# Kernel optimization log

Hardware: AMD Instinct MI355X
Metric: run time of the kernel (lower is better)

The kernel has to match this reference:

```python
import jax, jax.numpy as jnp
import numpy as np

DROPOUT_RATE = 0.6


def dropout(x, key, rate=DROPOUT_RATE):
    keep = jax.random.bernoulli(key, 1.0 - rate, x.shape)
    return jnp.where(keep, x / (1.0 - rate), 0.0).astype(x.dtype)


def gcn_conv(x, W, b, src, dst, n_nodes):
    # h = x @ W  (tiny linear), then symmetric-normalized scatter-add over edges
    h = x @ W                                             # [N, C_out]
    deg = jax.ops.segment_sum(jnp.ones_like(dst, dtype=h.dtype), dst,
                              num_segments=n_nodes)       # in-degree at targets
    dinv = jnp.where(deg > 0, jax.lax.rsqrt(jnp.maximum(deg, 1.0)), 0.0)
    norm = dinv[src] * dinv[dst]                          # [E]
    msg = h[src] * norm[:, None]                          # [E, C_out] gather
    out = jax.ops.segment_sum(msg, dst, num_segments=n_nodes)  # scatter-add
    return out + b


def setup_inputs() -> dict:
    key = jax.random.key(0)
    k_x, k_e, k_w1, k_w2 = jax.random.split(key, 4)
    N, E = 100000, 6400000
    x = jax.random.normal(k_x, (N, 1), dtype=jnp.float32)
    edge_index = jax.random.randint(k_e, (2, E), 0, N, dtype=jnp.int64)
    # GCNConv weights (glorot-ish scale) and zero biases
    W1 = jax.random.normal(k_w1, (1, 16), dtype=jnp.float32) * (1.0 / np.sqrt(1.0))
    b1 = jnp.zeros((16,), dtype=jnp.float32)
    W2 = jax.random.normal(k_w2, (16, 1), dtype=jnp.float32) * (1.0 / np.sqrt(16.0))
    b2 = jnp.zeros((1,), dtype=jnp.float32)
    return {"x": x, "edge_index": edge_index, "W1": W1, "b1": b1, "W2": W2, "b2": b2}


def reference(x, edge_index, W1, b1, W2, b2):
    n_nodes = x.shape[0]
    src, dst = edge_index[0], edge_index[1]
    k1, k2 = jax.random.split(jax.random.key(42), 2)
    h = dropout(x, k1)
    h = gcn_conv(h, W1, b1, src, dst, n_nodes)
    h = jax.nn.relu(h)
    h = dropout(h, k2)
    out = gcn_conv(h, W2, b2, src, dst, n_nodes)
    return out
```

## Files before the change

### kernel.cpp

```cpp
#include <hip/hip_runtime.h>
#include <hip/hip_bf16.h>
#include <stdint.h>


#define KEEP_P 0.4f
#define RANGE 2048
#define SHIFT 11
#define MASK 2047
#define BPC 1024
#define KS 32
#define SEGS (BPC / KS)
#define SPW (SEGS / 4)
#define NBMAX 64
#define TILE 2048
#define TILE4 (TILE / 4)

__host__ __device__ inline unsigned rotl32(unsigned v, int s) {
  return (v << s) | (v >> (32 - s));
}

__host__ __device__ inline void threefry2x32(unsigned key0, unsigned key1,
                                             unsigned x0, unsigned x1,
                                             unsigned& o0, unsigned& o1) {
  unsigned ks0 = key0, ks1 = key1, ks2 = key0 ^ key1 ^ 0x1BD11BDAu;
  unsigned v0 = x0 + ks0, v1 = x1 + ks1;
#define TF_R(r) { v0 += v1; v1 = rotl32(v1, r); v1 ^= v0; }
  TF_R(13) TF_R(15) TF_R(26) TF_R(6)
  v0 += ks1; v1 += ks2 + 1u;
  TF_R(17) TF_R(29) TF_R(16) TF_R(24)
  v0 += ks2; v1 += ks0 + 2u;
  TF_R(13) TF_R(15) TF_R(26) TF_R(6)
  v0 += ks0; v1 += ks1 + 3u;
  TF_R(17) TF_R(29) TF_R(16) TF_R(24)
  v0 += ks1; v1 += ks2 + 4u;
  TF_R(13) TF_R(15) TF_R(26) TF_R(6)
  v0 += ks2; v1 += ks0 + 5u;
#undef TF_R
  o0 = v0; o1 = v1;
}

__device__ inline float u01_from_bits(unsigned bits) {
  return __uint_as_float((bits >> 9) | 0x3f800000u) - 1.0f;
}

__global__ __launch_bounds__(256) void k_part(
    const int* __restrict__ src, const int* __restrict__ dst,
    unsigned* __restrict__ slots, unsigned* __restrict__ cnt,
    int NB, int CAP, int e4, int E) {
  __shared__ unsigned hist[NBMAX], scan_s[NBMAX + 1], off[NBMAX];
  __shared__ unsigned tbase[NBMAX], cur[NBMAX];
  __shared__ unsigned stage[TILE];
  __shared__ unsigned char stage_p[TILE];
  const int tid = threadIdx.x;
  const size_t blkbase = (size_t)blockIdx.x * NB;
  unsigned* myslots = slots + blkbase * CAP;
  for (int p = tid; p < NB; p += 256) cur[p] = (unsigned)(p * CAP);
  const int chunk = (e4 + BPC - 1) / BPC;
  const int j0 = blockIdx.x * chunk;
  const int j1 = min(j0 + chunk, e4);
  const int4* dst4 = reinterpret_cast<const int4*>(dst);
  const int4* src4 = reinterpret_cast<const int4*>(src);

  for (int t0 = j0; t0 < j1; t0 += TILE4) {
    __syncthreads();
    for (int p = tid; p < NB; p += 256) hist[p] = 0u;
    __syncthreads();
    const int ja = t0 + tid, jb = t0 + TILE4 / 2 + tid;
    const bool va = ja < j1 && tid < TILE4 / 2;
    const bool vb = jb < j1;
    int4 da, db;
    if (va) {
      da = dst4[ja];
      atomicAdd(&hist[(unsigned)da.x >> SHIFT], 1u);
      atomicAdd(&hist[(unsigned)da.y >> SHIFT], 1u);
      atomicAdd(&hist[(unsigned)da.z >> SHIFT], 1u);
      atomicAdd(&hist[(unsigned)da.w >> SHIFT], 1u);
    }
    if (vb) {
      db = dst4[jb];
      atomicAdd(&hist[(unsigned)db.x >> SHIFT], 1u);
      atomicAdd(&hist[(unsigned)db.y >> SHIFT], 1u);
      atomicAdd(&hist[(unsigned)db.z >> SHIFT], 1u);
      atomicAdd(&hist[(unsigned)db.w >> SHIFT], 1u);
    }
    __syncthreads();
    if (tid == 0) {
      unsigned acc = 0;
      for (int p = 0; p < NB; ++p) { scan_s[p] = acc; acc += hist[p]; }
      scan_s[NB] = acc;
    }
    __syncthreads();
    for (int p = tid; p < NB; p += 256) {
      off[p] = scan_s[p];
      tbase[p] = cur[p];
      cur[p] += hist[p];
    }
    __syncthreads();
#define STAGE1(d, s) { unsigned ud = (unsigned)(d), us = (unsigned)(s); \
    unsigned p = ud >> SHIFT; unsigned pos = atomicAdd(&off[p], 1u); \
    stage[pos] = (ud & MASK) | (us << SHIFT); stage_p[pos] = (unsigned char)p; }
    if (va) {
      int4 sa = src4[ja];
      STAGE1(da.x, sa.x) STAGE1(da.y, sa.y) STAGE1(da.z, sa.z) STAGE1(da.w, sa.w)
    }
    if (vb) {
      int4 sb = src4[jb];
      STAGE1(db.x, sb.x) STAGE1(db.y, sb.y) STAGE1(db.z, sb.z) STAGE1(db.w, sb.w)
    }
#undef STAGE1
    __syncthreads();
    const int tc = (int)scan_s[NB];
    for (int i = tid; i < tc; i += 256) {
      unsigned p = stage_p[i];
      myslots[tbase[p] + ((unsigned)i - scan_s[p])] = stage[i];
    }
  }
  __syncthreads();
  if (blockIdx.x == 0) {
    for (int t = e4 * 4 + tid; t < E; t += 256) {
      unsigned ud = (unsigned)dst[t], us = (unsigned)src[t];
      unsigned p = ud >> SHIFT;
      unsigned pos = atomicAdd(&cur[p], 1u);
      myslots[pos] = (ud & MASK) | (us << SHIFT);
    }
  }
  __syncthreads();
  for (int p = tid; p < NB; p += 256)
    cnt[blkbase + p] = cur[p] - (unsigned)(p * CAP);
}

__global__ __launch_bounds__(256) void k_deg2(
    const unsigned* __restrict__ slots, const unsigned* __restrict__ cnt,
    unsigned short* __restrict__ part16, int NB, int CAP) {
  __shared__ unsigned bins[RANGE / 2];
  const int tid = threadIdx.x, w = tid >> 6, lane = tid & 63;
  const int p = blockIdx.y, kd = blockIdx.x;
  for (int i = tid; i < RANGE / 2; i += 256) bins[i] = 0u;
  __syncthreads();
  int l[SPW]; const unsigned* e[SPW];
#pragma unroll
  for (int s = 0; s < SPW; ++s) {
    const int b = kd * SEGS + w * SPW + s;
    l[s] = cnt[(size_t)b * NB + p];
    e[s] = slots + ((size_t)b * NB + p) * CAP;
  }
  const int half = lane >> 5, li = lane & 31;
#define DEG_ONE(v) { unsigned r = (v) & MASK; \
    atomicAdd(&bins[r >> 1], 1u << ((r & 1) * 16)); }
#pragma unroll
  for (int r = 0; r < SPW / 2; ++r) {
    const int s = 2 * r + half;
    const unsigned* es = e[s];
    const int ls = l[s];
    const int i1 = 4 * li, i2 = 128 + 4 * li;
    const bool f1 = i1 + 4 <= ls, f2 = i2 + 4 <= ls;
    uint4 u1, u2;
    if (f1) u1 = *reinterpret_cast<const uint4*>(es + i1);
    if (f2) u2 = *reinterpret_cast<const uint4*>(es + i2);
    if (f1) { DEG_ONE(u1.x) DEG_ONE(u1.y) DEG_ONE(u1.z) DEG_ONE(u1.w) }
    if (f2) { DEG_ONE(u2.x) DEG_ONE(u2.y) DEG_ONE(u2.z) DEG_ONE(u2.w) }
  }
  if (lane < SPW) {
    const int s = lane;
    for (int k = l[s] & ~3; k < l[s]; ++k) DEG_ONE(e[s][k])
  }
#undef DEG_ONE
  __syncthreads();
  unsigned* my32 = (unsigned*)(part16 + ((size_t)kd * gridDim.y + p) * RANGE);
  for (int i = tid; i < RANGE / 2; i += 256) my32[i] = bins[i];
}

__global__ __launch_bounds__(256) void k_node1(
    const float* __restrict__ x, const unsigned short* __restrict__ part16,
    float* __restrict__ dinv, float* __restrict__ y,
    int NB, int n, unsigned k1a, unsigned k1b) {
  int i = blockIdx.x * blockDim.x + threadIdx.x;
  if (i >= n) return;
  const int p = i >> SHIFT, r = i & MASK;
  unsigned d = 0;
  for (int b = 0; b < KS; ++b)
    d += part16[((size_t)b * NB + p) * RANGE + r];
  float di = (d > 0) ? (1.0f / sqrtf((float)d)) : 0.0f;
  dinv[i] = di;
  unsigned o0, o1;
  threefry2x32(k1a, k1b, 0u, (unsigned)i, o0, o1);
  float u = u01_from_bits(o0 ^ o1);
  float xd = (u < KEEP_P) ? (x[i] / KEEP_P) : 0.0f;
  y[i] = xd * di;
}

__global__ __launch_bounds__(256) void k_scat(
    const unsigned* __restrict__ slots, const unsigned* __restrict__ cnt,
    const float* __restrict__ val, float* __restrict__ part,
    int NB, int CAP) {
  __shared__ float bins[RANGE];
  const int tid = threadIdx.x, w = tid >> 6, lane = tid & 63;
  const int p = blockIdx.y, ks = blockIdx.x;
  for (int i = tid; i < RANGE; i += 256) bins[i] = 0.0f;
  __syncthreads();
  int l[SPW]; const unsigned* e[SPW];
#pragma unroll
  for (int s = 0; s < SPW; ++s) {
    const int b = ks * SEGS + w * SPW + s;
    l[s] = cnt[(size_t)b * NB + p];
    e[s] = slots + ((size_t)b * NB + p) * CAP;
  }
  const int half = lane >> 5, li = lane & 31;
#pragma unroll
  for (int r = 0; r < SPW / 2; ++r) {
    const int s = 2 * r + half;
    const unsigned* es = e[s];
    const int ls = l[s];
    const int i1 = 4 * li, i2 = 128 + 4 * li;
    const bool f1 = i1 + 4 <= ls, f2 = i2 + 4 <= ls;
    uint4 u1, u2;
    if (f1) u1 = *reinterpret_cast<const uint4*>(es + i1);
    if (f2) u2 = *reinterpret_cast<const uint4*>(es + i2);
    float g0, g1, g2, g3, g4, g5, g6, g7;
    if (f1) {
      g0 = val[u1.x >> SHIFT]; g1 = val[u1.y >> SHIFT];
      g2 = val[u1.z >> SHIFT]; g3 = val[u1.w >> SHIFT];
    }
    if (f2) {
      g4 = val[u2.x >> SHIFT]; g5 = val[u2.y >> SHIFT];
      g6 = val[u2.z >> SHIFT]; g7 = val[u2.w >> SHIFT];
    }
    if (f1) {
      atomicAdd(&bins[u1.x & MASK], g0);
      atomicAdd(&bins[u1.y & MASK], g1);
      atomicAdd(&bins[u1.z & MASK], g2);
      atomicAdd(&bins[u1.w & MASK], g3);
    }
    if (f2) {
      atomicAdd(&bins[u2.x & MASK], g4);
      atomicAdd(&bins[u2.y & MASK], g5);
      atomicAdd(&bins[u2.z & MASK], g6);
      atomicAdd(&bins[u2.w & MASK], g7);
    }
  }
  if (lane < SPW) {
    const int s = lane;
    for (int k = l[s] & ~3; k < l[s]; ++k) {
      unsigned v = e[s][k];
      atomicAdd(&bins[v & MASK], val[v >> SHIFT]);
    }
  }
  __syncthreads();
  float* my = part + ((size_t)ks * NB + p) * RANGE;
  for (int i = tid; i < RANGE; i += 256) my[i] = bins[i];
}

__global__ __launch_bounds__(256) void k_node2(
    const float* __restrict__ part, const float* __restrict__ dinv,
    const float* __restrict__ W1, const float* __restrict__ b1,
    const float* __restrict__ W2, float* __restrict__ z2,
    int NB, int n, unsigned k2a, unsigned k2b) {
  int i = blockIdx.x * blockDim.x + threadIdx.x;
  if (i >= n) return;
  const int p = i >> SHIFT, r = i & MASK;
  float s = 0.0f;
  for (int b = 0; b < KS; ++b)
    s += part[((size_t)b * NB + p) * RANGE + r];
  float t = s * dinv[i];
  float z = 0.0f;
  unsigned base = (unsigned)i * 16u;
#pragma unroll
  for (int c = 0; c < 16; ++c) {
    float h = W1[c] * t + b1[c];
    h = fmaxf(h, 0.0f);
    unsigned o0, o1;
    threefry2x32(k2a, k2b, 0u, base + (unsigned)c, o0, o1);
    float u = u01_from_bits(o0 ^ o1);
    float hd = (u < KEEP_P) ? (h / KEEP_P) : 0.0f;
    z += hd * W2[c];
  }
  z2[i] = z * dinv[i];
}

__global__ __launch_bounds__(256) void k_final(
    const float* __restrict__ part, const float* __restrict__ dinv,
    const float* __restrict__ b2, float* __restrict__ out,
    int NB, int n) {
  int i = blockIdx.x * blockDim.x + threadIdx.x;
  if (i >= n) return;
  const int p = i >> SHIFT, r = i & MASK;
  float s = 0.0f;
  for (int b = 0; b < KS; ++b)
    s += part[((size_t)b * NB + p) * RANGE + r];
  out[i] = b2[0] + dinv[i] * s;
}

extern "C" void kernel_launch(void* const* d_in, const int* in_sizes, int n_in,
                              void* d_out, int out_size, void* d_ws, size_t ws_size,
                              hipStream_t stream) {
  const float* x  = (const float*)d_in[0];
  const int* edge = (const int*)d_in[1];
  const float* W1 = (const float*)d_in[2];
  const float* b1 = (const float*)d_in[3];
  const float* W2 = (const float*)d_in[4];
  const float* b2 = (const float*)d_in[5];
  float* out = (float*)d_out;

  const int N = in_sizes[0];
  const int E = in_sizes[1] / 2;
  const int* src = edge;
  const int* dst = edge + E;

  const int NP = (N + 255) & ~255;
  const int NB = (N + RANGE - 1) / RANGE;

  const size_t cnt_sz  = (size_t)BPC * NB * 4;
  const size_t part_sz = (size_t)KS * NB * RANGE * 4;
  const size_t small_sz = (size_t)3 * NP * 4;
  size_t fixed = cnt_sz + part_sz + small_sz + 512;
  size_t avail = ws_size > fixed ? ws_size - fixed : 0;
  int CAP = (int)(avail / ((size_t)NB * BPC * 4));
  CAP &= ~3;
  if (CAP > 208) CAP = 208;
  if (CAP < 176) CAP = 176;

  char* w = (char*)d_ws;
  unsigned* slots = (unsigned*)w;        w += (size_t)NB * BPC * CAP * 4;
  unsigned* cnt   = (unsigned*)w;        w += cnt_sz;
  w = (char*)(((uintptr_t)w + 255) & ~(uintptr_t)255);
  float* part_f = (float*)w;
  unsigned short* part16 = (unsigned short*)w;
  w += part_sz;
  float* dinv = (float*)w;
  float* y    = dinv + NP;
  float* z2   = y + NP;

  unsigned k1a, k1b, k2a, k2b;
  threefry2x32(0u, 42u, 0u, 0u, k1a, k1b);
  threefry2x32(0u, 42u, 0u, 1u, k2a, k2b);

  const int e4 = E >> 2;
  const int gN = (N + 255) / 256;

  k_part <<<BPC, 256, 0, stream>>>(src, dst, slots, cnt, NB, CAP, e4, E);
  k_deg2 <<<dim3(KS, NB), 256, 0, stream>>>(slots, cnt, part16, NB, CAP);
  k_node1<<<gN, 256, 0, stream>>>(x, part16, dinv, y, NB, N, k1a, k1b);
  k_scat <<<dim3(KS, NB), 256, 0, stream>>>(slots, cnt, y, part_f, NB, CAP);
  k_node2<<<gN, 256, 0, stream>>>(part_f, dinv, W1, b1, W2, z2, NB, N, k2a, k2b);
  k_scat <<<dim3(KS, NB), 256, 0, stream>>>(slots, cnt, z2, part_f, NB, CAP);
  k_final<<<gN, 256, 0, stream>>>(part_f, dinv, b2, out, NB, N);
}
```

Baseline: 223.4 us.

## Add second source-partition pass so scatter gathers node values from shared memory

Adds a second partitioning kernel that regroups the already dst-partitioned edges by source-node window (8192 nodes), writing them into per-(dst-bucket, src-window) slots. The scatter kernels can then stage the source values for one window in LDS and gather from shared memory instead of making random global loads. Degree counting also reads the new layout, and the serial prefix scan in k_part becomes a wave shuffle scan. The cost is an extra full pass over the edge list and more workspace, plus a statistically sized capacity CAP2 that silently drops edges if a bucket overflows.

```diff
diff --git a/kernel.cpp b/kernel.cpp
--- a/kernel.cpp
+++ b/kernel.cpp
@@ -1,6 +1,7 @@
 #include <hip/hip_runtime.h>
 #include <hip/hip_bf16.h>
 #include <stdint.h>
+#include <math.h>
 
 
 #define KEEP_P 0.4f
@@ -8,12 +9,12 @@
 #define SHIFT 11
 #define MASK 2047
 #define BPC 1024
-#define KS 32
-#define SEGS (BPC / KS)
-#define SPW (SEGS / 4)
 #define NBMAX 64
 #define TILE 2048
 #define TILE4 (TILE / 4)
+#define G16 16
+#define ST2 3456
+#define SL 8192
 
 __host__ __device__ inline unsigned rotl32(unsigned v, int s) {
   return (v << s) | (v >> (32 - s));
@@ -46,12 +47,15 @@
 __global__ __launch_bounds__(256) void k_part(
     const int* __restrict__ src, const int* __restrict__ dst,
     unsigned* __restrict__ slots, unsigned* __restrict__ cnt,
-    int NB, int CAP, int e4, int E) {
+    int NB, int CAP, int e4, int E,
+    unsigned* __restrict__ cur2, int nz) {
   __shared__ unsigned hist[NBMAX], scan_s[NBMAX + 1], off[NBMAX];
   __shared__ unsigned tbase[NBMAX], cur[NBMAX];
   __shared__ unsigned stage[TILE];
   __shared__ unsigned char stage_p[TILE];
   const int tid = threadIdx.x;
+  if (blockIdx.x == 0)
+    for (int i = tid; i < nz; i += 256) cur2[i] = 0u;
   const size_t blkbase = (size_t)blockIdx.x * NB;
   unsigned* myslots = slots + blkbase * CAP;
   for (int p = tid; p < NB; p += 256) cur[p] = (unsigned)(p * CAP);
@@ -84,16 +88,22 @@
       atomicAdd(&hist[(unsigned)db.w >> SHIFT], 1u);
     }
     __syncthreads();
-    if (tid == 0) {
-      unsigned acc = 0;
-      for (int p = 0; p < NB; ++p) { scan_s[p] = acc; acc += hist[p]; }
-      scan_s[NB] = acc;
-    }
-    __syncthreads();
-    for (int p = tid; p < NB; p += 256) {
-      off[p] = scan_s[p];
-      tbase[p] = cur[p];
-      cur[p] += hist[p];
+    if (tid < 64) {
+      unsigned h = (tid < NB) ? hist[tid] : 0u;
+      unsigned inc = h;
+#pragma unroll
+      for (int d = 1; d < 64; d <<= 1) {
+        unsigned t = __shfl_up(inc, d, 64);
+        if (tid >= d) inc += t;
+      }
+      if (tid < NB) {
+        unsigned ex = inc - h;
+        scan_s[tid] = ex;
+        off[tid] = ex;
+        tbase[tid] = cur[tid];
+        cur[tid] += h;
+      }
+      if (tid == NB - 1) scan_s[NB] = inc;
     }
     __syncthreads();
 #define STAGE1(d, s) { unsigned ud = (unsigned)(d), us = (unsigned)(s); \
@@ -129,56 +139,112 @@
     cnt[blkbase + p] = cur[p] - (unsigned)(p * CAP);
 }
 
-__global__ __launch_bounds__(256) void k_deg2(
+__global__ __launch_bounds__(256) void k_part2(
     const unsigned* __restrict__ slots, const unsigned* __restrict__ cnt,
-    unsigned short* __restrict__ part16, int NB, int CAP) {
+    unsigned* __restrict__ slots2, unsigned* __restrict__ cur2,
+    int NB, int CAP, int NS, int CAP2) {
+  __shared__ unsigned raw[ST2], stage[ST2];
+  __shared__ unsigned char tagp[ST2];
+  __shared__ unsigned lens_s[G16], offs_s[G16];
+  __shared__ unsigned hist[16], scan_s[16], off[16], gbase[16];
+  __shared__ unsigned tc_s;
+  const int tid = threadIdx.x, wv = tid >> 6, lane = tid & 63;
+  const int p = blockIdx.x, g = blockIdx.y;
+  if (tid < 16) hist[tid] = 0u;
+  if (tid < 64) {
+    unsigned ln = 0;
+    if (lane < G16) {
+      int b = g * G16 + lane;
+      ln = cnt[(size_t)b * NB + p];
+      if (ln > (unsigned)CAP) ln = (unsigned)CAP;
+      lens_s[lane] = ln;
+    }
+    unsigned inc = ln;
+#pragma unroll
+    for (int d = 1; d < 16; d <<= 1) {
+      unsigned t = __shfl_up(inc, d, 64);
+      if (lane >= d) inc += t;
+    }
+    if (lane < G16) offs_s[lane] = inc - ln;
+    if (lane == G16 - 1) tc_s = inc;
+  }
+  __syncthreads();
+  for (int k = 0; k < 4; ++k) {
+    const int j = 4 * wv + k;
+    const unsigned len = lens_s[j], off0 = offs_s[j];
+    const unsigned* e = slots + ((size_t)(g * G16 + j) * NB + p) * CAP;
+    for (unsigned i = lane; i < len; i += 64) raw[off0 + i] = e[i];
+  }
+  __syncthreads();
+  const int TC = (int)tc_s;
+  for (int i = tid; i < TC; i += 256)
+    atomicAdd(&hist[raw[i] >> 24], 1u);
+  __syncthreads();
+  if (tid < 64) {
+    unsigned h = (lane < NS) ? hist[lane] : 0u;
+    unsigned inc = h;
+#pragma unroll
+    for (int d = 1; d < 16; d <<= 1) {
+      unsigned t = __shfl_up(inc, d, 64);
+      if (lane >= d) inc += t;
+    }
+    if (lane < NS) {
+      scan_s[lane] = inc - h;
+      off[lane] = inc - h;
+      gbase[lane] = atomicAdd(&cur2[p * NS + lane], h);
+    }
+  }
+  __syncthreads();
+  for (int i = tid; i < TC; i += 256) {
+    unsigned v = raw[i];
+    unsigned s = v >> 24;
+    unsigned pos = atomicAdd(&off[s], 1u);
+    stage[pos] = (v & MASK) | (((v >> SHIFT) & (SL - 1)) << SHIFT);
+    tagp[pos] = (unsigned char)s;
+  }
+  __syncthreads();
+  for (int i = tid; i < TC; i += 256) {
+    unsigned s = tagp[i];
+    unsigned idx = gbase[s] + ((unsigned)i - scan_s[s]);
+    if (idx < (unsigned)CAP2)
+      slots2[(size_t)(p * NS + (int)s) * CAP2 + idx] = stage[i];
+  }
+}
+
+__global__ __launch_bounds__(256) void k_deg3(
+    const unsigned* __restrict__ slots2, const unsigned* __restrict__ cnt2,
+    unsigned short* __restrict__ part16, int NB, int NS, int CAP2) {
   __shared__ unsigned bins[RANGE / 2];
-  const int tid = threadIdx.x, w = tid >> 6, lane = tid & 63;
-  const int p = blockIdx.y, kd = blockIdx.x;
+  const int tid = threadIdx.x;
+  const int sh = blockIdx.x, p = blockIdx.y;
+  const int s = sh >> 1, h = sh & 1;
   for (int i = tid; i < RANGE / 2; i += 256) bins[i] = 0u;
   __syncthreads();
-  int l[SPW]; const unsigned* e[SPW];
-#pragma unroll
-  for (int s = 0; s < SPW; ++s) {
-    const int b = kd * SEGS + w * SPW + s;
-    l[s] = cnt[(size_t)b * NB + p];
-    e[s] = slots + ((size_t)b * NB + p) * CAP;
-  }
-  const int half = lane >> 5, li = lane & 31;
+  const int c = p * NS + s;
+  int len = cnt2[c]; if (len > CAP2) len = CAP2;
+  const unsigned* e = slots2 + (size_t)c * CAP2;
 #define DEG_ONE(v) { unsigned r = (v) & MASK; \
     atomicAdd(&bins[r >> 1], 1u << ((r & 1) * 16)); }
-#pragma unroll
-  for (int r = 0; r < SPW / 2; ++r) {
-    const int s = 2 * r + half;
-    const unsigned* es = e[s];
-    const int ls = l[s];
-    const int i1 = 4 * li, i2 = 128 + 4 * li;
-    const bool f1 = i1 + 4 <= ls, f2 = i2 + 4 <= ls;
-    uint4 u1, u2;
-    if (f1) u1 = *reinterpret_cast<const uint4*>(es + i1);
-    if (f2) u2 = *reinterpret_cast<const uint4*>(es + i2);
-    if (f1) { DEG_ONE(u1.x) DEG_ONE(u1.y) DEG_ONE(u1.z) DEG_ONE(u1.w) }
-    if (f2) { DEG_ONE(u2.x) DEG_ONE(u2.y) DEG_ONE(u2.z) DEG_ONE(u2.w) }
-  }
-  if (lane < SPW) {
-    const int s = lane;
-    for (int k = l[s] & ~3; k < l[s]; ++k) DEG_ONE(e[s][k])
-  }
+  for (int i = (h * 256 + tid) * 4; i + 4 <= len; i += 2048) {
+    uint4 u = *reinterpret_cast<const uint4*>(e + i);
+    DEG_ONE(u.x) DEG_ONE(u.y) DEG_ONE(u.z) DEG_ONE(u.w)
+  }
+  if (h == 0 && tid < (len & 3)) DEG_ONE(e[(len & ~3) + tid])
 #undef DEG_ONE
   __syncthreads();
-  unsigned* my32 = (unsigned*)(part16 + ((size_t)kd * gridDim.y + p) * RANGE);
+  unsigned* my32 = (unsigned*)(part16 + ((size_t)sh * NB + p) * RANGE);
   for (int i = tid; i < RANGE / 2; i += 256) my32[i] = bins[i];
 }
 
 __global__ __launch_bounds__(256) void k_node1(
     const float* __restrict__ x, const unsigned short* __restrict__ part16,
     float* __restrict__ dinv, float* __restrict__ y,
-    int NB, int n, unsigned k1a, unsigned k1b) {
+    int NB, int np, int n, unsigned k1a, unsigned k1b) {
   int i = blockIdx.x * blockDim.x + threadIdx.x;
   if (i >= n) return;
   const int p = i >> SHIFT, r = i & MASK;
   unsigned d = 0;
-  for (int b = 0; b < KS; ++b)
+  for (int b = 0; b < np; ++b)
     d += part16[((size_t)b * NB + p) * RANGE + r];
   float di = (d > 0) ? (1.0f / sqrtf((float)d)) : 0.0f;
   dinv[i] = di;
@@ -189,64 +255,45 @@
   y[i] = xd * di;
 }
 
-__global__ __launch_bounds__(256) void k_scat(
-    const unsigned* __restrict__ slots, const unsigned* __restrict__ cnt,
+__global__ __launch_bounds__(256) void k_scat2(
+    const unsigned* __restrict__ slots2, const unsigned* __restrict__ cnt2,
     const float* __restrict__ val, float* __restrict__ part,
-    int NB, int CAP) {
+    int NB, int NS, int CAP2, int n) {
+  __shared__ float vs[SL];
   __shared__ float bins[RANGE];
-  const int tid = threadIdx.x, w = tid >> 6, lane = tid & 63;
-  const int p = blockIdx.y, ks = blockIdx.x;
+  const int tid = threadIdx.x;
+  const int sh = blockIdx.x, p = blockIdx.y;
+  const int s = sh >> 1, h = sh & 1;
+  const int base_n = s * SL;
+  const int lim = n - base_n;
+  if (lim >= SL) {
+    const float4* v4 = reinterpret_cast<const float4*>(val + base_n);
+    float4* s4 = reinterpret_cast<float4*>(vs);
+    for (int i = tid; i < SL / 4; i += 256) s4[i] = v4[i];
+  } else {
+    for (int i = tid; i < SL; i += 256)
+      vs[i] = (i < lim) ? val[base_n + i] : 0.0f;
+  }
   for (int i = tid; i < RANGE; i += 256) bins[i] = 0.0f;
   __syncthreads();
-  int l[SPW]; const unsigned* e[SPW];
-#pragma unroll
-  for (int s = 0; s < SPW; ++s) {
-    const int b = ks * SEGS + w * SPW + s;
-    l[s] = cnt[(size_t)b * NB + p];
-    e[s] = slots + ((size_t)b * NB + p) * CAP;
-  }
-  const int half = lane >> 5, li = lane & 31;
-#pragma unroll
-  for (int r = 0; r < SPW / 2; ++r) {
-    const int s = 2 * r + half;
-    const unsigned* es = e[s];
-    const int ls = l[s];
-    const int i1 = 4 * li, i2 = 128 + 4 * li;
-    const bool f1 = i1 + 4 <= ls, f2 = i2 + 4 <= ls;
-    uint4 u1, u2;
-    if (f1) u1 = *reinterpret_cast<const uint4*>(es + i1);
-    if (f2) u2 = *reinterpret_cast<const uint4*>(es + i2);
-    float g0, g1, g2, g3, g4, g5, g6, g7;
-    if (f1) {
-      g0 = val[u1.x >> SHIFT]; g1 = val[u1.y >> SHIFT];
-      g2 = val[u1.z >> SHIFT]; g3 = val[u1.w >> SHIFT];
-    }
-    if (f2) {
-      g4 = val[u2.x >> SHIFT]; g5 = val[u2.y >> SHIFT];
-      g6 = val[u2.z >> SHIFT]; g7 = val[u2.w >> SHIFT];
-    }
-    if (f1) {
-      atomicAdd(&bins[u1.x & MASK], g0);
-      atomicAdd(&bins[u1.y & MASK], g1);
-      atomicAdd(&bins[u1.z & MASK], g2);
-      atomicAdd(&bins[u1.w & MASK], g3);
-    }
-    if (f2) {
-      atomicAdd(&bins[u2.x & MASK], g4);
-      atomicAdd(&bins[u2.y & MASK], g5);
-      atomicAdd(&bins[u2.z & MASK], g6);
-      atomicAdd(&bins[u2.w & MASK], g7);
-    }
-  }
-  if (lane < SPW) {
-    const int s = lane;
-    for (int k = l[s] & ~3; k < l[s]; ++k) {
-      unsigned v = e[s][k];
-      atomicAdd(&bins[v & MASK], val[v >> SHIFT]);
-    }
-  }
-  __syncthreads();
-  float* my = part + ((size_t)ks * NB + p) * RANGE;
+  const int c = p * NS + s;
+  int len = cnt2[c]; if (len > CAP2) len = CAP2;
+  const unsigned* e = slots2 + (size_t)c * CAP2;
+  for (int i = (h * 256 + tid) * 4; i + 4 <= len; i += 2048) {
+    uint4 u = *reinterpret_cast<const uint4*>(e + i);
+    float a0 = vs[u.x >> SHIFT], a1 = vs[u.y >> SHIFT];
+    float a2 = vs[u.z >> SHIFT], a3 = vs[u.w >> SHIFT];
+    atomicAdd(&bins[u.x & MASK], a0);
+    atomicAdd(&bins[u.y & MASK], a1);
+    atomicAdd(&bins[u.z & MASK], a2);
+    atomicAdd(&bins[u.w & MASK], a3);
+  }
+  if (h == 0 && tid < (len & 3)) {
+    unsigned v = e[(len & ~3) + tid];
+    atomicAdd(&bins[v & MASK], vs[v >> SHIFT]);
+  }
+  __syncthreads();
+  float* my = part + ((size_t)sh * NB + p) * RANGE;
   for (int i = tid; i < RANGE; i += 256) my[i] = bins[i];
 }
 
@@ -254,12 +301,12 @@
     const float* __restrict__ part, const float* __restrict__ dinv,
     const float* __restrict__ W1, const float* __restrict__ b1,
     const float* __restrict__ W2, float* __restrict__ z2,
-    int NB, int n, unsigned k2a, unsigned k2b) {
+    int NB, int np, int n, unsigned k2a, unsigned k2b) {
   int i = blockIdx.x * blockDim.x + threadIdx.x;
   if (i >= n) return;
   const int p = i >> SHIFT, r = i & MASK;
   float s = 0.0f;
-  for (int b = 0; b < KS; ++b)
+  for (int b = 0; b < np; ++b)
     s += part[((size_t)b * NB + p) * RANGE + r];
   float t = s * dinv[i];
   float z = 0.0f;
@@ -280,12 +327,12 @@
 __global__ __launch_bounds__(256) void k_final(
     const float* __restrict__ part, const float* __restrict__ dinv,
     const float* __restrict__ b2, float* __restrict__ out,
-    int NB, int n) {
+    int NB, int np, int n) {
   int i = blockIdx.x * blockDim.x + threadIdx.x;
   if (i >= n) return;
   const int p = i >> SHIFT, r = i & MASK;
   float s = 0.0f;
-  for (int b = 0; b < KS; ++b)
+  for (int b = 0; b < np; ++b)
     s += part[((size_t)b * NB + p) * RANGE + r];
   out[i] = b2[0] + dinv[i] * s;
 }
@@ -308,11 +355,19 @@
 
   const int NP = (N + 255) & ~255;
   const int NB = (N + RANGE - 1) / RANGE;
-
-  const size_t cnt_sz  = (size_t)BPC * NB * 4;
-  const size_t part_sz = (size_t)KS * NB * RANGE * 4;
+  const int NS = (N + SL - 1) / SL;
+  const int np2 = 2 * NS;
+
+  double lam2 = (double)E * (double)RANGE * (double)SL / ((double)N * (double)N);
+  int CAP2 = (int)(lam2 + 7.0 * sqrt(lam2)) + 8;
+  CAP2 = (CAP2 + 3) & ~3;
+
+  const size_t cnt_sz   = (size_t)BPC * NB * 4;
+  const size_t cur2_sz  = ((size_t)NB * NS * 4 + 255) & ~(size_t)255;
+  const size_t slots2_sz= (size_t)NB * NS * CAP2 * 4;
+  const size_t part_sz  = (size_t)np2 * NB * RANGE * 4;
   const size_t small_sz = (size_t)3 * NP * 4;
-  size_t fixed = cnt_sz + part_sz + small_sz + 512;
+  size_t fixed = cnt_sz + cur2_sz + slots2_sz + part_sz + small_sz + 1024;
   size_t avail = ws_size > fixed ? ws_size - fixed : 0;
   int CAP = (int)(avail / ((size_t)NB * BPC * 4));
   CAP &= ~3;
@@ -320,8 +375,11 @@
   if (CAP < 176) CAP = 176;
 
   char* w = (char*)d_ws;
-  unsigned* slots = (unsigned*)w;        w += (size_t)NB * BPC * CAP * 4;
-  unsigned* cnt   = (unsigned*)w;        w += cnt_sz;
+  unsigned* slots  = (unsigned*)w;  w += (size_t)NB * BPC * CAP * 4;
+  unsigned* cnt    = (unsigned*)w;  w += cnt_sz;
+  w = (char*)(((uintptr_t)w + 255) & ~(uintptr_t)255);
+  unsigned* cur2   = (unsigned*)w;  w += cur2_sz;
+  unsigned* slots2 = (unsigned*)w;  w += slots2_sz;
   w = (char*)(((uintptr_t)w + 255) & ~(uintptr_t)255);
   float* part_f = (float*)w;
   unsigned short* part16 = (unsigned short*)w;
@@ -337,11 +395,17 @@
   const int e4 = E >> 2;
   const int gN = (N + 255) / 256;
 
-  k_part <<<BPC, 256, 0, stream>>>(src, dst, slots, cnt, NB, CAP, e4, E);
-  k_deg2 <<<dim3(KS, NB), 256, 0, stream>>>(slots, cnt, part16, NB, CAP);
-  k_node1<<<gN, 256, 0, stream>>>(x, part16, dinv, y, NB, N, k1a, k1b);
-  k_scat <<<dim3(KS, NB), 256, 0, stream>>>(slots, cnt, y, part_f, NB, CAP);
-  k_node2<<<gN, 256, 0, stream>>>(part_f, dinv, W1, b1, W2, z2, NB, N, k2a, k2b);
-  k_scat <<<dim3(KS, NB), 256, 0, stream>>>(slots, cnt, z2, part_f, NB, CAP);
-  k_final<<<gN, 256, 0, stream>>>(part_f, dinv, b2, out, NB, N);
-}
+  k_part <<<BPC, 256, 0, stream>>>(src, dst, slots, cnt, NB, CAP, e4, E,
+                                   cur2, NB * NS);
+  k_part2<<<dim3(NB, BPC / G16), 256, 0, stream>>>(slots, cnt, slots2, cur2,
+                                                   NB, CAP, NS, CAP2);
+  k_deg3 <<<dim3(np2, NB), 256, 0, stream>>>(slots2, cur2, part16, NB, NS, CAP2);
+  k_node1<<<gN, 256, 0, stream>>>(x, part16, dinv, y, NB, np2, N, k1a, k1b);
+  k_scat2<<<dim3(np2, NB), 256, 0, stream>>>(slots2, cur2, y, part_f,
+                                             NB, NS, CAP2, N);
+  k_node2<<<gN, 256, 0, stream>>>(part_f, dinv, W1, b1, W2, z2, NB, np2, N,
+                                  k2a, k2b);
+  k_scat2<<<dim3(np2, NB), 256, 0, stream>>>(slots2, cur2, z2, part_f,
+                                             NB, NS, CAP2, N);
+  k_final<<<gN, 256, 0, stream>>>(part_f, dinv, b2, out, NB, np2, N);
+}
```

After: 261.9 us. 17.2% more time.
